# Kernel optimization log

Hardware: AMD Instinct MI355X
Metric: run time of the kernel (lower is better)

Reference implementation:

```python
import jax, jax.numpy as jnp
import numpy as np

L_SEQ = 2048
RECEPTIVE = 128  # band half-width
B, H, D = 2, 16, 64


def _band_mask(l, r, dtype):
    i = jnp.arange(l)
    return (jnp.abs(i[:, None] - i[None, :]) <= r).astype(dtype)


def setup_inputs() -> dict:
    key = jax.random.key(0)
    kq, kk = jax.random.split(key)
    queries = jax.random.normal(kq, (B, H, L_SEQ, D), dtype=jnp.float32)
    keys = jax.random.normal(kk, (B, H, L_SEQ, D), dtype=jnp.float32)
    return {"queries": queries, "keys": keys}


def reference(queries, keys):
    # Original: sum_d( q[...,i,None,d] * mask[i,j] * k[...,None,j,d] )
    # Mask is independent of d, so this equals (Q @ K^T) * band_mask.
    band = _band_mask(queries.shape[-2], RECEPTIVE, queries.dtype)  # [L, L]
    scores = jnp.einsum('bhid,bhjd->bhij', queries, keys)  # [B, H, L, L]
    return scores * band
```

## Files before the change

kernel.cpp:

```cpp
#include <hip/hip_runtime.h>


constexpr int L = 2048;
constexpr int D = 64;
constexpr int R = 128;
constexpr int TILE = 64;
constexpr int NT = L / TILE;
constexpr int KS = D + 1;

__global__ __launch_bounds__(256, 4)
void receptive_attention_kernel(const float* __restrict__ q,
                                const float* __restrict__ k,
                                float* __restrict__ out) {
    const int ti   = blockIdx.x;
    const int kind = blockIdx.y;
    const int bh   = blockIdx.z;
    const int t    = threadIdx.x;

    const int jt_lo = (ti - 2 > 0) ? (ti - 2) : 0;
    const int jt_hi = (ti + 2 < NT - 1) ? (ti + 2) : (NT - 1);

    float* outStrip = out + (size_t)bh * L * L + (size_t)ti * TILE * L;

    __shared__ float Qs[TILE * KS];
    __shared__ float Ks[TILE * KS];

    if (kind >= 5) {
        const int r0  = (kind - 5) * 16;
        const int wl4 = (jt_lo * TILE) / 4;
        const int rb  = (jt_hi + 1) * TILE;
        const int nz4 = (L - (jt_hi - jt_lo + 1) * TILE) / 4;
        const float4 z = make_float4(0.f, 0.f, 0.f, 0.f);
        for (int r = 0; r < 16; ++r) {
            float* orow = outStrip + (size_t)(r0 + r) * L;
            for (int f = t; f < nz4; f += 256) {
                int col = (f < wl4) ? (f * 4) : (rb + (f - wl4) * 4);
                *reinterpret_cast<float4*>(orow + col) = z;
            }
        }
        return;
    }

    const int tj = ti + kind - 2;
    if (tj < 0 || tj >= NT) return;

    const float* qTile = q + ((size_t)bh * L + (size_t)ti * TILE) * D;
    const float* kTile = k + ((size_t)bh * L + (size_t)tj * TILE) * D;

    #pragma unroll
    for (int it = 0; it < 4; ++it) {
        int idx = t + it * 256;
        int row = idx >> 4;
        int col = (idx & 15) * 4;
        float4 qv = *reinterpret_cast<const float4*>(qTile + row * D + col);
        float4 kv = *reinterpret_cast<const float4*>(kTile + row * D + col);
        float* qd = &Qs[row * KS + col];
        qd[0] = qv.x; qd[1] = qv.y; qd[2] = qv.z; qd[3] = qv.w;
        float* kd = &Ks[row * KS + col];
        kd[0] = kv.x; kd[1] = kv.y; kd[2] = kv.z; kd[3] = kv.w;
    }
    __syncthreads();

    const int tr = (t >> 4) * 4;
    const int tc = (t & 15) * 4;

    float acc[4][4] = {};
    #pragma unroll 8
    for (int d = 0; d < D; ++d) {
        float a0 = Qs[(tr + 0) * KS + d];
        float a1 = Qs[(tr + 1) * KS + d];
        float a2 = Qs[(tr + 2) * KS + d];
        float a3 = Qs[(tr + 3) * KS + d];
        float b0 = Ks[(tc + 0) * KS + d];
        float b1 = Ks[(tc + 1) * KS + d];
        float b2 = Ks[(tc + 2) * KS + d];
        float b3 = Ks[(tc + 3) * KS + d];
        acc[0][0] += a0 * b0; acc[0][1] += a0 * b1; acc[0][2] += a0 * b2; acc[0][3] += a0 * b3;
        acc[1][0] += a1 * b0; acc[1][1] += a1 * b1; acc[1][2] += a1 * b2; acc[1][3] += a1 * b3;
        acc[2][0] += a2 * b0; acc[2][1] += a2 * b1; acc[2][2] += a2 * b2; acc[2][3] += a2 * b3;
        acc[3][0] += a3 * b0; acc[3][1] += a3 * b1; acc[3][2] += a3 * b2; acc[3][3] += a3 * b3;
    }

    float* outTile = outStrip + tj * TILE;
    const int gi0 = ti * TILE + tr;
    const int gj0 = tj * TILE + tc;
    #pragma unroll
    for (int rr = 0; rr < 4; ++rr) {
        int gi = gi0 + rr;
        float4 v;
        float* vp = &v.x;
        #pragma unroll
        for (int cc = 0; cc < 4; ++cc) {
            int gj = gj0 + cc;
            int diff = gi - gj;
            if (diff < 0) diff = -diff;
            vp[cc] = (diff <= R) ? acc[rr][cc] : 0.f;
        }
        *reinterpret_cast<float4*>(outTile + (size_t)(tr + rr) * L + tc) = v;
    }
}

extern "C" void kernel_launch(void* const* d_in, const int* in_sizes, int n_in,
                              void* d_out, int out_size, void* d_ws, size_t ws_size,
                              hipStream_t stream) {
    const float* q = (const float*)d_in[0];
    const float* k = (const float*)d_in[1];
    float* out = (float*)d_out;

    dim3 grid(NT, 9, 32);
    receptive_attention_kernel<<<grid, 256, 0, stream>>>(q, k, out);
}
```

Baseline: 554.7 us.

## Process whole band strip per 1024-thread block with Q reuse and K prefetch

```diff
diff --git a/kernel.cpp b/kernel.cpp
--- a/kernel.cpp
+++ b/kernel.cpp
@@ -7,96 +7,158 @@
 constexpr int TILE = 64;
 constexpr int NT = L / TILE;
 constexpr int KS = D + 1;
+constexpr int BAND_W = 5 * TILE;
+constexpr int ARENA = 3 * TILE * KS;
 
-__global__ __launch_bounds__(256, 4)
+__global__ __launch_bounds__(1024, 4)
 void receptive_attention_kernel(const float* __restrict__ q,
                                 const float* __restrict__ k,
                                 float* __restrict__ out) {
-    const int ti   = blockIdx.x;
-    const int kind = blockIdx.y;
-    const int bh   = blockIdx.z;
-    const int t    = threadIdx.x;
+    const int ti = blockIdx.x;
+    const int bh = blockIdx.z;
+    const int t  = threadIdx.x;
 
     const int jt_lo = (ti - 2 > 0) ? (ti - 2) : 0;
     const int jt_hi = (ti + 2 < NT - 1) ? (ti + 2) : (NT - 1);
+    const int ntj   = jt_hi - jt_lo + 1;
+    const int c0    = jt_lo * TILE;
 
     float* outStrip = out + (size_t)bh * L * L + (size_t)ti * TILE * L;
 
-    __shared__ float Qs[TILE * KS];
-    __shared__ float Ks[TILE * KS];
-
-    if (kind >= 5) {
-        const int r0  = (kind - 5) * 16;
-        const int wl4 = (jt_lo * TILE) / 4;
-        const int rb  = (jt_hi + 1) * TILE;
-        const int nz4 = (L - (jt_hi - jt_lo + 1) * TILE) / 4;
+    if (blockIdx.y == 1) {
+        const int wl4 = jt_lo * 16;
+        const int wr4 = (NT - 1 - jt_hi) * 16;
+        const int rb4 = (jt_hi + 1) * 16;
         const float4 z = make_float4(0.f, 0.f, 0.f, 0.f);
-        for (int r = 0; r < 16; ++r) {
-            float* orow = outStrip + (size_t)(r0 + r) * L;
-            for (int f = t; f < nz4; f += 256) {
-                int col = (f < wl4) ? (f * 4) : (rb + (f - wl4) * 4);
-                *reinterpret_cast<float4*>(orow + col) = z;
+        for (int r = 0; r < TILE; ++r) {
+            float* orow = outStrip + (size_t)r * L;
+            if (t < wl4) {
+                *reinterpret_cast<float4*>(orow + t * 4) = z;
+            } else if (t >= 512 && (t - 512) < wr4) {
+                *reinterpret_cast<float4*>(orow + (rb4 + (t - 512)) * 4) = z;
             }
         }
         return;
     }
 
-    const int tj = ti + kind - 2;
-    if (tj < 0 || tj >= NT) return;
+    __shared__ __align__(16) float smem[ARENA];
+
+    float* Qs = smem;
+    const int s = t & 511;
+    const int g = t >> 9;
+    float* Kb = smem + TILE * KS + g * TILE * KS;
 
     const float* qTile = q + ((size_t)bh * L + (size_t)ti * TILE) * D;
-    const float* kTile = k + ((size_t)bh * L + (size_t)tj * TILE) * D;
+    const float* kBase = k + ((size_t)bh * L + (size_t)jt_lo * TILE) * D;
 
-    #pragma unroll
-    for (int it = 0; it < 4; ++it) {
-        int idx = t + it * 256;
-        int row = idx >> 4;
-        int col = (idx & 15) * 4;
+    {
+        const int row = t >> 4;
+        const int col = (t & 15) * 4;
         float4 qv = *reinterpret_cast<const float4*>(qTile + row * D + col);
-        float4 kv = *reinterpret_cast<const float4*>(kTile + row * D + col);
+
+        const int kr = s >> 4;
+        const int kc = (s & 15) * 4;
+        const float* kt = kBase + (size_t)g * TILE * D;
+        float4 ka = *reinterpret_cast<const float4*>(kt + kr * D + kc);
+        float4 kb = *reinterpret_cast<const float4*>(kt + (kr + 32) * D + kc);
+
         float* qd = &Qs[row * KS + col];
         qd[0] = qv.x; qd[1] = qv.y; qd[2] = qv.z; qd[3] = qv.w;
-        float* kd = &Ks[row * KS + col];
-        kd[0] = kv.x; kd[1] = kv.y; kd[2] = kv.z; kd[3] = kv.w;
+        float* kd0 = &Kb[kr * KS + kc];
+        kd0[0] = ka.x; kd0[1] = ka.y; kd0[2] = ka.z; kd0[3] = ka.w;
+        float* kd1 = &Kb[(kr + 32) * KS + kc];
+        kd1[0] = kb.x; kd1[1] = kb.y; kd1[2] = kb.z; kd1[3] = kb.w;
     }
     __syncthreads();
 
-    const int tr = (t >> 4) * 4;
-    const int tc = (t & 15) * 4;
+    const int tr  = (s >> 5) * 4;
+    const int tc2 = (s & 31) * 2;
 
-    float acc[4][4] = {};
-    #pragma unroll 8
-    for (int d = 0; d < D; ++d) {
-        float a0 = Qs[(tr + 0) * KS + d];
-        float a1 = Qs[(tr + 1) * KS + d];
-        float a2 = Qs[(tr + 2) * KS + d];
-        float a3 = Qs[(tr + 3) * KS + d];
-        float b0 = Ks[(tc + 0) * KS + d];
-        float b1 = Ks[(tc + 1) * KS + d];
-        float b2 = Ks[(tc + 2) * KS + d];
-        float b3 = Ks[(tc + 3) * KS + d];
-        acc[0][0] += a0 * b0; acc[0][1] += a0 * b1; acc[0][2] += a0 * b2; acc[0][3] += a0 * b3;
-        acc[1][0] += a1 * b0; acc[1][1] += a1 * b1; acc[1][2] += a1 * b2; acc[1][3] += a1 * b3;
-        acc[2][0] += a2 * b0; acc[2][1] += a2 * b1; acc[2][2] += a2 * b2; acc[2][3] += a2 * b3;
-        acc[3][0] += a3 * b0; acc[3][1] += a3 * b1; acc[3][2] += a3 * b2; acc[3][3] += a3 * b3;
+    float acc[3][4][2] = {};
+
+    #pragma unroll
+    for (int p = 0; p < 3; ++p) {
+        float4 na, nb;
+        const int ntt = 2 * (p + 1) + g;
+        const bool npv = (p < 2) && (ntt < ntj);
+        if (npv) {
+            const float* kt = kBase + (size_t)ntt * TILE * D;
+            const int kr = s >> 4;
+            const int kc = (s & 15) * 4;
+            na = *reinterpret_cast<const float4*>(kt + kr * D + kc);
+            nb = *reinterpret_cast<const float4*>(kt + (kr + 32) * D + kc);
+        }
+
+        const int tt = 2 * p + g;
+        if (tt < ntj) {
+            #pragma unroll 8
+            for (int d = 0; d < D; ++d) {
+                float q0 = Qs[(tr + 0) * KS + d];
+                float q1 = Qs[(tr + 1) * KS + d];
+                float q2 = Qs[(tr + 2) * KS + d];
+                float q3 = Qs[(tr + 3) * KS + d];
+                float k0 = Kb[(tc2 + 0) * KS + d];
+                float k1 = Kb[(tc2 + 1) * KS + d];
+                acc[p][0][0] += q0 * k0; acc[p][0][1] += q0 * k1;
+                acc[p][1][0] += q1 * k0; acc[p][1][1] += q1 * k1;
+                acc[p][2][0] += q2 * k0; acc[p][2][1] += q2 * k1;
+                acc[p][3][0] += q3 * k0; acc[p][3][1] += q3 * k1;
+            }
+        }
+        __syncthreads();
+        if (npv) {
+            const int kr = s >> 4;
+            const int kc = (s & 15) * 4;
+            float* kd0 = &Kb[kr * KS + kc];
+            kd0[0] = na.x; kd0[1] = na.y; kd0[2] = na.z; kd0[3] = na.w;
+            float* kd1 = &Kb[(kr + 32) * KS + kc];
+            kd1[0] = nb.x; kd1[1] = nb.y; kd1[2] = nb.z; kd1[3] = nb.w;
+        }
+        __syncthreads();
     }
 
-    float* outTile = outStrip + tj * TILE;
+    float* Band = smem;
     const int gi0 = ti * TILE + tr;
-    const int gj0 = tj * TILE + tc;
+    const int bw4 = ntj * 16;
+
     #pragma unroll
-    for (int rr = 0; rr < 4; ++rr) {
-        int gi = gi0 + rr;
-        float4 v;
-        float* vp = &v.x;
+    for (int half = 0; half < 2; ++half) {
+        const int rlo = half * 32;
+        if (tr >= rlo && tr < rlo + 32) {
+            #pragma unroll
+            for (int p = 0; p < 3; ++p) {
+                const int tt = 2 * p + g;
+                if (tt < ntj) {
+                    const int gj0 = (jt_lo + tt) * TILE + tc2;
+                    #pragma unroll
+                    for (int i = 0; i < 4; ++i) {
+                        int d0 = gi0 + i - gj0;       if (d0 < 0) d0 = -d0;
+                        int d1 = gi0 + i - (gj0 + 1); if (d1 < 0) d1 = -d1;
+                        float2 v;
+                        v.x = (d0 <= R) ? acc[p][i][0] : 0.f;
+                        v.y = (d1 <= R) ? acc[p][i][1] : 0.f;
+                        *reinterpret_cast<float2*>(
+                            &Band[(tr - rlo + i) * BAND_W + tt * TILE + tc2]) = v;
+                    }
+                }
+            }
+        }
+        __syncthreads();
+
         #pragma unroll
-        for (int cc = 0; cc < 4; ++cc) {
-            int gj = gj0 + cc;
-            int diff = gi - gj;
-            if (diff < 0) diff = -diff;
-            vp[cc] = (diff <= R) ? acc[rr][cc] : 0.f;
+        for (int it = 0; it < 3; ++it) {
+            const int f = t + it * 1024;
+            if (f < 2560) {
+                const int row = f / 80;
+                const int c4  = f - row * 80;
+                if (c4 < bw4) {
+                    float4 v = *reinterpret_cast<float4*>(&Band[row * BAND_W + c4 * 4]);
+                    *reinterpret_cast<float4*>(
+                        outStrip + (size_t)(rlo + row) * L + c0 + c4 * 4) = v;
+                }
+            }
         }
-        *reinterpret_cast<float4*>(outTile + (size_t)(tr + rr) * L + tc) = v;
+        __syncthreads();
     }
 }
 
@@ -107,6 +169,6 @@
     const float* k = (const float*)d_in[1];
     float* out = (float*)d_out;
 
-    dim3 grid(NT, 9, 32);
-    receptive_attention_kernel<<<grid, 256, 0, stream>>>(q, k, out);
+    dim3 grid(NT, 2, 32);
+    receptive_attention_kernel<<<grid, 1024, 0, stream>>>(q, k, out);
 }
```

After: 567.3 us. 2.3% more time.

## Use XOR-swizzled float4 shared-memory layout and interleave zero-fill with compute blocks

Applied to the files above, without the earlier changes.

```diff
diff --git a/kernel.cpp b/kernel.cpp
--- a/kernel.cpp
+++ b/kernel.cpp
@@ -6,24 +6,22 @@
 constexpr int R = 128;
 constexpr int TILE = 64;
 constexpr int NT = L / TILE;
-constexpr int KS = D + 1;
 
 __global__ __launch_bounds__(256, 4)
 void receptive_attention_kernel(const float* __restrict__ q,
                                 const float* __restrict__ k,
                                 float* __restrict__ out) {
-    const int ti   = blockIdx.x;
-    const int kind = blockIdx.y;
-    const int bh   = blockIdx.z;
-    const int t    = threadIdx.x;
+    const int ti = blockIdx.x;
+    const int y  = blockIdx.y;
+    const int bh = blockIdx.z;
+    const int t  = threadIdx.x;
+
+    const int kind = (y & 1) ? (5 + (y >> 1)) : (y >> 1);
 
     const int jt_lo = (ti - 2 > 0) ? (ti - 2) : 0;
     const int jt_hi = (ti + 2 < NT - 1) ? (ti + 2) : (NT - 1);
 
     float* outStrip = out + (size_t)bh * L * L + (size_t)ti * TILE * L;
-
-    __shared__ float Qs[TILE * KS];
-    __shared__ float Ks[TILE * KS];
 
     if (kind >= 5) {
         const int r0  = (kind - 5) * 16;
@@ -44,41 +42,52 @@
     const int tj = ti + kind - 2;
     if (tj < 0 || tj >= NT) return;
 
+    __shared__ __align__(16) float Qs[TILE * 64];
+    __shared__ __align__(16) float Ks[TILE * 64];
+
     const float* qTile = q + ((size_t)bh * L + (size_t)ti * TILE) * D;
     const float* kTile = k + ((size_t)bh * L + (size_t)tj * TILE) * D;
 
     #pragma unroll
     for (int it = 0; it < 4; ++it) {
-        int idx = t + it * 256;
-        int row = idx >> 4;
-        int col = (idx & 15) * 4;
-        float4 qv = *reinterpret_cast<const float4*>(qTile + row * D + col);
-        float4 kv = *reinterpret_cast<const float4*>(kTile + row * D + col);
-        float* qd = &Qs[row * KS + col];
-        qd[0] = qv.x; qd[1] = qv.y; qd[2] = qv.z; qd[3] = qv.w;
-        float* kd = &Ks[row * KS + col];
-        kd[0] = kv.x; kd[1] = kv.y; kd[2] = kv.z; kd[3] = kv.w;
+        int idx  = t + it * 256;
+        int row  = idx >> 4;
+        int col4 = idx & 15;
+        float4 qv = *reinterpret_cast<const float4*>(qTile + row * D + col4 * 4);
+        float4 kv = *reinterpret_cast<const float4*>(kTile + row * D + col4 * 4);
+        int wblk = (col4 ^ (row >> 2)) & 15;
+        *reinterpret_cast<float4*>(&Qs[row * 64 + wblk * 4]) = qv;
+        *reinterpret_cast<float4*>(&Ks[row * 64 + wblk * 4]) = kv;
     }
     __syncthreads();
 
     const int tr = (t >> 4) * 4;
     const int tc = (t & 15) * 4;
+    const int xq = (t >> 4) & 15;
+    const int xk = t & 15;
 
     float acc[4][4] = {};
-    #pragma unroll 8
-    for (int d = 0; d < D; ++d) {
-        float a0 = Qs[(tr + 0) * KS + d];
-        float a1 = Qs[(tr + 1) * KS + d];
-        float a2 = Qs[(tr + 2) * KS + d];
-        float a3 = Qs[(tr + 3) * KS + d];
-        float b0 = Ks[(tc + 0) * KS + d];
-        float b1 = Ks[(tc + 1) * KS + d];
-        float b2 = Ks[(tc + 2) * KS + d];
-        float b3 = Ks[(tc + 3) * KS + d];
-        acc[0][0] += a0 * b0; acc[0][1] += a0 * b1; acc[0][2] += a0 * b2; acc[0][3] += a0 * b3;
-        acc[1][0] += a1 * b0; acc[1][1] += a1 * b1; acc[1][2] += a1 * b2; acc[1][3] += a1 * b3;
-        acc[2][0] += a2 * b0; acc[2][1] += a2 * b1; acc[2][2] += a2 * b2; acc[2][3] += a2 * b3;
-        acc[3][0] += a3 * b0; acc[3][1] += a3 * b1; acc[3][2] += a3 * b2; acc[3][3] += a3 * b3;
+    #pragma unroll 4
+    for (int b = 0; b < 16; ++b) {
+        float4 qv[4], kv[4];
+        const int qb = ((b ^ xq) & 15) * 4;
+        const int kb = ((b ^ xk) & 15) * 4;
+        #pragma unroll
+        for (int r = 0; r < 4; ++r)
+            qv[r] = *reinterpret_cast<const float4*>(&Qs[(tr + r) * 64 + qb]);
+        #pragma unroll
+        for (int c = 0; c < 4; ++c)
+            kv[c] = *reinterpret_cast<const float4*>(&Ks[(tc + c) * 64 + kb]);
+        #pragma unroll
+        for (int rr = 0; rr < 4; ++rr) {
+            #pragma unroll
+            for (int cc = 0; cc < 4; ++cc) {
+                acc[rr][cc] += qv[rr].x * kv[cc].x;
+                acc[rr][cc] += qv[rr].y * kv[cc].y;
+                acc[rr][cc] += qv[rr].z * kv[cc].z;
+                acc[rr][cc] += qv[rr].w * kv[cc].w;
+            }
+        }
     }
 
     float* outTile = outStrip + tj * TILE;
```

Result: no change. 552.5 us (-0.4%).
